# Kernel optimization log

Hardware: AMD Instinct MI355X
Metric: run time of the kernel (lower is better)

The kernel has to match this reference:

```python
import jax, jax.numpy as jnp
import numpy as np

B, S, N_CATE, N_CONT = 32, 1024, 4, 4
HIDDEN, ATTN, VOCAB, EMB = 1024, 512, 1000, 128


def sinusoidal_pe(seq_len, d_model, base=10000.0):
    pos = jnp.arange(seq_len, dtype=jnp.float32)[:, None]            # [S,1]
    i = jnp.arange(d_model // 2, dtype=jnp.float32)[None, :]         # [1,D/2]
    ang = pos / jnp.power(base, 2.0 * i / d_model)                   # [S,D/2]
    pe = jnp.zeros((seq_len, d_model), dtype=jnp.float32)
    pe = pe.at[:, 0::2].set(jnp.sin(ang))
    pe = pe.at[:, 1::2].set(jnp.cos(ang))
    return pe


def setup_inputs() -> dict:
    key = jax.random.key(0)
    ks = jax.random.split(key, 20)
    s = 0.02
    inp = {
        "cate_x": jax.random.randint(ks[0], (B, S, N_CATE), 0, VOCAB, dtype=jnp.int64)
                  if jax.config.read("jax_enable_x64") else
                  jax.random.randint(ks[0], (B, S, N_CATE), 0, VOCAB, dtype=jnp.int32),
        "cont_x": jax.random.normal(ks[1], (B, S, N_CONT), dtype=jnp.float32),
        "mask": jnp.ones((B, S), dtype=bool),
        "targets": jax.random.uniform(ks[2], (B, S), dtype=jnp.float32),
        # EntireEmbedding params: 4 cate tables + cont linear + comb projection
        "E0": jax.random.normal(ks[3], (VOCAB, EMB), dtype=jnp.float32) * s,
        "E1": jax.random.normal(ks[4], (VOCAB, EMB), dtype=jnp.float32) * s,
        "E2": jax.random.normal(ks[5], (VOCAB, EMB), dtype=jnp.float32) * s,
        "E3": jax.random.normal(ks[6], (VOCAB, EMB), dtype=jnp.float32) * s,
        "Wc": jax.random.normal(ks[7], (N_CONT, N_CATE * EMB), dtype=jnp.float32) * s,
        "Wproj": jax.random.normal(ks[8], (2 * N_CATE * EMB, HIDDEN), dtype=jnp.float32) * s,
        # two-head attention linears (bias=False)
        "WQ1": jax.random.normal(ks[9], (HIDDEN, ATTN), dtype=jnp.float32) * s,
        "WK1": jax.random.normal(ks[10], (HIDDEN, ATTN), dtype=jnp.float32) * s,
        "WV1": jax.random.normal(ks[11], (HIDDEN, ATTN), dtype=jnp.float32) * s,
        "WQ2": jax.random.normal(ks[12], (HIDDEN, ATTN), dtype=jnp.float32) * s,
        "WK2": jax.random.normal(ks[13], (HIDDEN, ATTN), dtype=jnp.float32) * s,
        "WV2": jax.random.normal(ks[14], (HIDDEN, ATTN), dtype=jnp.float32) * s,
        "W0": jax.random.normal(ks[15], (2 * ATTN, HIDDEN), dtype=jnp.float32) * s,
        "Wf": jax.random.normal(ks[16], (HIDDEN, 1), dtype=jnp.float32) * s,
    }
    return inp


def _attend(x, WQ, WK, WV):
    Q = x @ WQ  # [B,S,A]
    K = x @ WK
    V = x @ WV
    scores = jnp.einsum("bqd,bkd->bqk", Q, K) / jnp.sqrt(jnp.float32(ATTN))
    # faithful to nn.Softmax(dim=1): normalize over the QUERY axis
    attn = jax.nn.softmax(scores, axis=1)
    return jnp.einsum("bqk,bkv->bqv", attn, V)


def reference(cate_x, cont_x, mask, targets, E0, E1, E2, E3, Wc, Wproj,
              WQ1, WK1, WV1, WQ2, WK2, WV2, W0, Wf):
    # EntireEmbedding: per-feature cate embeddings + cont projection -> comb proj
    cate_emb = jnp.concatenate(
        [E0[cate_x[..., 0]], E1[cate_x[..., 1]], E2[cate_x[..., 2]], E3[cate_x[..., 3]]],
        axis=-1)                                   # [B,S,512]
    cont_emb = cont_x @ Wc                          # [B,S,512]
    x = jnp.concatenate([cate_emb, cont_emb], axis=-1) @ Wproj  # [B,S,H]
    x = x + sinusoidal_pe(x.shape[1], HIDDEN)[None, :, :]
    z1 = _attend(x, WQ1, WK1, WV1)                  # [B,S,A]
    z2 = _attend(x, WQ2, WK2, WV2)                  # [B,S,A]
    z = jnp.concatenate([z1, z2], axis=-1) @ W0     # [B,S,H]
    out = jax.nn.sigmoid(z @ Wf)                    # FinalConnecting: Linear(H,1)+sigmoid
    return out.squeeze(-1)                          # [B,S]
```

## Files before the change

kernel.cpp:

```cpp
#include <hip/hip_runtime.h>
#include <hip/hip_bf16.h>
#include <math.h>

#define BB    32
#define SS    1024
#define HID   1024
#define AT    512
#define NVOC  1000
#define NT    (BB*SS)

typedef unsigned short u16;
typedef __attribute__((ext_vector_type(8))) short s16x8;
typedef __attribute__((ext_vector_type(4))) float f32x4;

__device__ __forceinline__ float bf2f(u16 u) {
    union { unsigned int i; float f; } x; x.i = ((unsigned int)u) << 16; return x.f;
}
__device__ __forceinline__ u16 f2bf(float f) {
    union { float f; unsigned int i; } u; u.f = f;
    unsigned int r = u.i + 0x7fffu + ((u.i >> 16) & 1u);
    return (u16)(r >> 16);
}
__device__ __forceinline__ float4 ld4(const float* p) { return *(const float4*)p; }
__device__ __forceinline__ float4 ld4bf(const u16* p) {
    ushort4 v = *(const ushort4*)p;
    return make_float4(bf2f(v.x), bf2f(v.y), bf2f(v.z), bf2f(v.w));
}
__device__ __forceinline__ void unpack8(uint4 v, float* x) {
    x[0] = bf2f((u16)(v.x & 0xffff)); x[1] = bf2f((u16)(v.x >> 16));
    x[2] = bf2f((u16)(v.y & 0xffff)); x[3] = bf2f((u16)(v.y >> 16));
    x[4] = bf2f((u16)(v.z & 0xffff)); x[5] = bf2f((u16)(v.z >> 16));
    x[6] = bf2f((u16)(v.w & 0xffff)); x[7] = bf2f((u16)(v.w >> 16));
}

__device__ __forceinline__ void gld16(const u16* g, u16* l) {
    __builtin_amdgcn_global_load_lds(
        (const __attribute__((address_space(1))) unsigned int*)g,
        (__attribute__((address_space(3))) unsigned int*)l,
        16, 0, 0);
}

struct Ptrs4f { const float* p[4]; };

__device__ __forceinline__ float blockReduceSum(float x) {
    #pragma unroll
    for (int off = 32; off > 0; off >>= 1) x += __shfl_down(x, off, 64);
    __shared__ float tmp[4];
    int lane = threadIdx.x & 63, wid = threadIdx.x >> 6;
    if (lane == 0) tmp[wid] = x;
    __syncthreads();
    if (threadIdx.x == 0) x = tmp[0] + tmp[1] + tmp[2] + tmp[3];
    return x;
}
__device__ __forceinline__ float waveReduceSum(float x) {
    #pragma unroll
    for (int off = 32; off > 0; off >>= 1) x += __shfl_down(x, off, 64);
    return x;
}

__global__ void k_s1(Ptrs4f E, const float* __restrict__ Wproj, Ptrs4f W,
                     const float* __restrict__ W0, const float* __restrict__ Wf,
                     u16* __restrict__ PE16, u16* __restrict__ E16o, u16* __restrict__ Wp16,
                     u16* __restrict__ Wt, float* __restrict__ W0f,
                     float* __restrict__ Wcp, float* __restrict__ CQ) {
    int blk = blockIdx.x, tid = threadIdx.x;
    if (blk < 2048) {
        int idx = blk*256 + tid;
        int s = idx >> 9, i = idx & 511;
        const float l2_10000 = 13.287712379549449f;
        float denom = exp2f((2.f * (float)i / 1024.f) * l2_10000);
        float ang = (float)s / denom;
        unsigned int pack = ((unsigned int)f2bf(cosf(ang)) << 16) | f2bf(sinf(ang));
        *(unsigned int*)(PE16 + (size_t)s*1024 + 2*i) = pack;
    } else if (blk < 4048) {
        int id2 = blk - 2048;
        int f = id2 / 500;
        int i = (id2 % 500)*256 + tid;
        E16o[(size_t)f*128000 + i] = f2bf(E.p[f][i]);
    } else if (blk < 6096) {
        int i = (blk - 4048)*256 + tid;
        Wp16[i] = f2bf(Wproj[i]);
    } else if (blk < 8144) {
        int tb = blk - 6096;
        int mat = tb >> 9, t2 = tb & 511;
        int cx = t2 & 15, ry = t2 >> 4;
        int r0 = ry*32, c0 = cx*32;
        const float* in = W.p[mat];
        u16* out = Wt + (size_t)mat*1024*512;
        __shared__ float tt[32][33];
        int tx = tid & 31, ty8 = tid >> 5;
        #pragma unroll
        for (int it = 0; it < 4; ++it)
            tt[ty8 + it*8][tx] = in[(size_t)(r0 + ty8 + it*8)*512 + c0 + tx];
        __syncthreads();
        #pragma unroll
        for (int it = 0; it < 4; ++it)
            out[(size_t)(c0 + ty8 + it*8)*1024 + r0 + tx] = f2bf(tt[tx][ty8 + it*8]);
    } else if (blk < 9168) {
        int row = blk - 8144;
        const float* rp = W0 + (size_t)row*1024;
        float a = 0.f;
        for (int j = tid; j < 1024; j += 256) a += rp[j] * Wf[j];
        a = blockReduceSum(a);
        if (tid == 0) W0f[row] = a;
    } else {
        int idx = (blk - 9168)*256 + tid;
        if (idx < 4096) Wcp[idx] = 0.f;
        else CQ[idx - 4096] = 0.f;
    }
}

__global__ void k_s2(const float* __restrict__ Wc, const float* __restrict__ Wproj,
                     Ptrs4f W, const float* __restrict__ WV1, const float* __restrict__ WV2,
                     const float* __restrict__ W0f, float* __restrict__ Wcp, float* __restrict__ v) {
    int blk = blockIdx.x, tid = threadIdx.x;
    if (blk < 64) {
        int c = blk >> 4, ic = (blk >> 2) & 3, jc = blk & 3;
        int i = ic*256 + tid;
        float a = 0.f;
        for (int j = jc*128; j < jc*128 + 128; ++j)
            a += Wc[c*512 + j] * Wproj[(size_t)(512 + j)*1024 + i];
        atomicAdd(&Wcp[c*1024 + i], a);
    } else {
        int b2 = blk - 64;
        int h = b2 >> 10, i = b2 & 1023;
        const float* WV = h ? WV2 : WV1;
        const float* wf = W0f + h*512;
        float a = 0.f;
        for (int aa = tid; aa < 512; aa += 256) a += WV[(size_t)i*512 + aa] * wf[aa];
        a = blockReduceSum(a);
        if (tid == 0) v[h*1024 + i] = a;
    }
}

__device__ __forceinline__ void cstore(float* p, float v) { *p = v; }
__device__ __forceinline__ void cstore(u16* p, float v)   { *p = f2bf(v); }

template<typename CT, bool STATS, bool CTRANS>
__device__ __forceinline__ void mfma_gemm(const u16* __restrict__ A, const u16* __restrict__ B,
                                          CT* __restrict__ C, int M, int N, int K, float alpha,
                                          float* __restrict__ Pm, float* __restrict__ Pd,
                                          int m0, int n0) {
    __shared__ u16 As[128*64];
    __shared__ u16 Bs[128*64];
    const int tid = threadIdx.x;
    const int wave = tid >> 6, lane = tid & 63;
    const int quad = lane >> 4, l16 = lane & 15;
    const int wm = (wave >> 1)*64, wn = (wave & 1)*64;
    const int srow = lane >> 3;
    const int scol = ((lane & 7) ^ srow) * 8;
    f32x4 acc[4][4] = {};

    for (int k0 = 0; k0 < K; k0 += 64) {
        #pragma unroll
        for (int p = 0; p < 4; ++p) {
            int rb = wave*32 + p*8;
            gld16(A + (size_t)(m0 + rb + srow)*K + k0 + scol, As + rb*64);
            gld16(B + (size_t)(n0 + rb + srow)*K + k0 + scol, Bs + rb*64);
        }
        __syncthreads();
        #pragma unroll
        for (int kk = 0; kk < 2; ++kk) {
            s16x8 af[4], bf[4];
            #pragma unroll
            for (int i = 0; i < 4; ++i) {
                int row = wm + i*16 + l16;
                af[i] = *(const s16x8*)(As + row*64 + (((kk*4 + quad) ^ (row & 7)) * 8));
            }
            #pragma unroll
            for (int j = 0; j < 4; ++j) {
                int row = wn + j*16 + l16;
                bf[j] = *(const s16x8*)(Bs + row*64 + (((kk*4 + quad) ^ (row & 7)) * 8));
            }
            #pragma unroll
            for (int i = 0; i < 4; ++i)
                #pragma unroll
                for (int j = 0; j < 4; ++j)
                    acc[i][j] = __builtin_amdgcn_mfma_f32_16x16x32_bf16(af[i], bf[j], acc[i][j], 0, 0, 0);
        }
        __syncthreads();
    }
    if (STATS) {
        #pragma unroll
        for (int i = 0; i < 4; ++i)
            #pragma unroll
            for (int r = 0; r < 4; ++r) {
                int gm = m0 + wm + i*16 + quad*4 + r;
                u16 b0 = f2bf(acc[i][0][r] * alpha);
                u16 b1 = f2bf(acc[i][1][r] * alpha);
                u16 b2 = f2bf(acc[i][2][r] * alpha);
                u16 b3 = f2bf(acc[i][3][r] * alpha);
                acc[i][0][r] = bf2f(b0); acc[i][1][r] = bf2f(b1);
                acc[i][2][r] = bf2f(b2); acc[i][3][r] = bf2f(b3);
                unsigned int lo = (unsigned int)b0 | ((unsigned int)b1 << 16);
                unsigned int hi = (unsigned int)b2 | ((unsigned int)b3 << 16);
                *(uint2*)((u16*)C + (size_t)gm*N + n0 + wn + l16*4) = make_uint2(lo, hi);
            }
        __shared__ float sMax[4][64];
        __shared__ float sSum[4][64];
        #pragma unroll
        for (int j = 0; j < 4; ++j) {
            float mx = -3.4e38f;
            #pragma unroll
            for (int i = 0; i < 4; ++i)
                #pragma unroll
                for (int r = 0; r < 4; ++r) mx = fmaxf(mx, acc[i][j][r]);
            mx = fmaxf(mx, __shfl_xor(mx, 16, 64));
            mx = fmaxf(mx, __shfl_xor(mx, 32, 64));
            float sm = 0.f;
            #pragma unroll
            for (int i = 0; i < 4; ++i)
                #pragma unroll
                for (int r = 0; r < 4; ++r) sm += exp2f(acc[i][j][r] - mx);
            sm += __shfl_xor(sm, 16, 64);
            sm += __shfl_xor(sm, 32, 64);
            if (quad == 0) { sMax[wave][j*16 + l16] = mx; sSum[wave][j*16 + l16] = sm; }
        }
        __syncthreads();
        if (tid < 128) {
            int c = tid;
            int w0 = (c < 64) ? 0 : 1, ci = c & 63;
            float m0v = sMax[w0][ci],     s0 = sSum[w0][ci];
            float m1v = sMax[w0 + 2][ci], s1 = sSum[w0 + 2][ci];
            float mm = fmaxf(m0v, m1v);
            float ss = s0 * exp2f(m0v - mm) + s1 * exp2f(m1v - mm);
            Pm[n0 + c] = mm;
            Pd[n0 + c] = ss;
        }
    } else {
        #pragma unroll
        for (int i = 0; i < 4; ++i) {
            #pragma unroll
            for (int r = 0; r < 4; ++r) {
                int gm = m0 + wm + i*16 + quad*4 + r;
                if (gm < M) {
                    #pragma unroll
                    for (int j = 0; j < 4; ++j) {
                        int gn = n0 + wn + j*16 + l16;
                        if (CTRANS) cstore(C + (size_t)gn*M + gm, acc[i][j][r] * alpha);
                        else        cstore(C + (size_t)gm*N + gn, acc[i][j][r] * alpha);
                    }
                }
            }
        }
    }
}

__global__ __launch_bounds__(256) void k_s3(const u16* __restrict__ Wp16, const u16* __restrict__ Wt,
                                            u16* __restrict__ PWT,
                                            Ptrs4f W, const float* __restrict__ Wcp, float* __restrict__ CQ,
                                            const float* __restrict__ Wproj, const float* __restrict__ v,
                                            float* __restrict__ pv) {
    int blk = blockIdx.x, tid = threadIdx.x;
    if (blk < 64) {
        int x = blk & 3, z = blk >> 2;
        int f = z >> 2, w = z & 3;
        mfma_gemm<u16,false,true>(Wp16 + (size_t)f*128*1024, Wt + (size_t)w*512*1024,
                                  PWT + (size_t)z*512*128, 128, 512, 1024, 1.f,
                                  nullptr, nullptr, 0, x*128);
    } else if (blk < 320) {
        int r = blk - 64;
        int ns = r & 1, wc = (r >> 1) & 15, jc = r >> 5;
        int w = wc & 3, c = wc >> 2; int n = ns*256 + tid;
        const float* Ww = W.p[w];
        float a = 0.f;
        for (int j = jc*128; j < jc*128 + 128; ++j) a += Wcp[c*1024 + j] * Ww[(size_t)j*512 + n];
        atomicAdd(&CQ[(size_t)(w*4 + c)*512 + n], a);
    } else {
        int b2 = blk - 320;
        int i = b2 & 127, fh = b2 >> 7; int f = fh >> 1, h = fh & 1;
        const float* row = Wproj + (size_t)(f*128 + i)*1024;
        const float* vh = v + h*1024;
        float a = 0.f;
        for (int j = tid; j < 1024; j += 256) a += row[j] * vh[j];
        a = blockReduceSum(a);
        if (tid == 0) pv[(size_t)fh*128 + i] = a;
    }
}

__global__ __launch_bounds__(256) void k_s4(const u16* __restrict__ E16, const u16* __restrict__ PWT,
                                            const u16* __restrict__ PE16, const u16* __restrict__ Wt,
                                            u16* __restrict__ TQK16, u16* __restrict__ PEQ16,
                                            const float* __restrict__ Wcp, const float* __restrict__ v,
                                            const float* __restrict__ pv,
                                            float* __restrict__ Ut, float* __restrict__ pu, float* __restrict__ cu) {
    int blk = blockIdx.x;
    if (blk < 640) {
        int z = blk >> 5, r = blk & 31, y = r >> 2, x = r & 3;
        if (z < 16) {
            int f = z >> 2;
            mfma_gemm<u16,false,false>(E16 + (size_t)f*128000, PWT + (size_t)z*512*128,
                       TQK16 + (size_t)z*1000*512, 1000, 512, 128, 1.f, nullptr, nullptr,
                       y*128, x*128);
        } else {
            int w = z - 16;
            mfma_gemm<u16,false,false>(PE16, Wt + (size_t)w*512*1024, PEQ16 + (size_t)w*1024*512,
                       1024, 512, 1024, 1.f, nullptr, nullptr, y*128, x*128);
        }
        return;
    }
    int id = blk - 640;
    if (id < 2000) {
        int wave = threadIdx.x >> 6, lane = threadIdx.x & 63;
        int d = id*4 + wave;
        int f = d / 2000, h = (d / 1000) & 1, r = d % 1000;
        unsigned int e2 = *(const unsigned int*)(E16 + ((size_t)f*1000 + r)*128 + lane*2);
        const float* pvp = pv + (size_t)(f*2 + h)*128 + lane*2;
        float a = bf2f((u16)(e2 & 0xffff)) * pvp[0] + bf2f((u16)(e2 >> 16)) * pvp[1];
        a = waveReduceSum(a);
        if (lane == 0) Ut[(size_t)(f*2 + h)*1000 + r] = a;
    } else if (id < 4048) {
        int tq = id - 2000; int h = tq >> 10, s = tq & 1023;
        float4 a = ld4bf(PE16 + (size_t)s*1024 + threadIdx.x*4);
        float4 b = ld4(v + h*1024 + threadIdx.x*4);
        float p = a.x*b.x + a.y*b.y + a.z*b.z + a.w*b.w;
        p = blockReduceSum(p);
        if (threadIdx.x == 0) pu[h*1024 + s] = p;
    } else {
        int tq = id - 4048; int h = tq >> 2, c = tq & 3;
        float4 a = ld4(Wcp + c*1024 + threadIdx.x*4);
        float4 b = ld4(v + h*1024 + threadIdx.x*4);
        float p = a.x*b.x + a.y*b.y + a.z*b.z + a.w*b.w;
        p = blockReduceSum(p);
        if (threadIdx.x == 0) cu[h*4 + c] = p;
    }
}

__global__ __launch_bounds__(256, 6) void k_g_S(const u16* __restrict__ Q, const u16* __restrict__ K,
                                             u16* __restrict__ Sb, float alpha,
                                             float* __restrict__ Pm, float* __restrict__ Pd, int b0) {
    size_t b = blockIdx.z;
    int bx = (blockIdx.x % 4)*2 + (blockIdx.y % 2);
    int by = (blockIdx.x / 4)*4 + (blockIdx.y / 2);
    size_t po = ((b0 + b)*8 + by)*1024;
    mfma_gemm<u16,true,false>(Q + b*SS*AT, K + b*SS*AT, Sb + b*SS*SS, 1024, 1024, 512, alpha,
                        Pm + po, Pd + po, by*128, bx*128);
}

__global__ void k_gather(const int* __restrict__ cate, const float* __restrict__ cont,
                         const u16* __restrict__ TQK, const float* __restrict__ CQ,
                         const u16* __restrict__ PEQ, const float* __restrict__ Ut,
                         const float* __restrict__ cu, const float* __restrict__ pu,
                         u16* __restrict__ Qh, u16* __restrict__ Kh,
                         float* __restrict__ u, int h) {
    int tid = threadIdx.x;
    size_t t = (size_t)blockIdx.x*2 + (tid >> 7);
    int r = tid & 127;
    int s = (int)(t & 1023);
    int4 cc = *(const int4*)(cate + t*4);
    float4 cv = ld4(cont + t*4);
    int e = r >> 6;
    int w = 2*h + e;
    int n = (r & 63)*8;
    const u16* t0 = TQK + ((size_t)(0*4  + w)*1000 + cc.x)*512 + n;
    const u16* t1 = TQK + ((size_t)(1*4  + w)*1000 + cc.y)*512 + n;
    const u16* t2 = TQK + ((size_t)(2*4  + w)*1000 + cc.z)*512 + n;
    const u16* t3 = TQK + ((size_t)(3*4  + w)*1000 + cc.w)*512 + n;
    const u16* pq = PEQ + ((size_t)w*1024 + s)*512 + n;
    const float* cq = CQ + (size_t)w*2048 + n;
    float a0[8], a1[8], a2[8], a3[8], ap[8];
    unpack8(*(const uint4*)t0, a0); unpack8(*(const uint4*)t1, a1);
    unpack8(*(const uint4*)t2, a2); unpack8(*(const uint4*)t3, a3);
    unpack8(*(const uint4*)pq, ap);
    unsigned int pack[4];
    #pragma unroll
    for (int jp = 0; jp < 4; ++jp) {
        float x0, x1;
        #pragma unroll
        for (int half = 0; half < 2; ++half) {
            int j = jp*2 + half;
            float x = a0[j] + a1[j] + a2[j] + a3[j] + ap[j]
                    + cv.x*cq[j] + cv.y*cq[512+j] + cv.z*cq[1024+j] + cv.w*cq[1536+j];
            if (half == 0) x0 = x; else x1 = x;
        }
        pack[jp] = ((unsigned int)f2bf(x1) << 16) | f2bf(x0);
    }
    u16* op = (e ? Kh : Qh) + t*512 + n;
    *(uint4*)op = make_uint4(pack[0], pack[1], pack[2], pack[3]);
    if (r == 0) {
        float uu = pu[h*1024 + s]
                 + Ut[(0*2 + h)*1000 + cc.x] + Ut[(1*2 + h)*1000 + cc.y]
                 + Ut[(2*2 + h)*1000 + cc.z] + Ut[(3*2 + h)*1000 + cc.w]
                 + cv.x*cu[h*4+0] + cv.y*cu[h*4+1] + cv.z*cu[h*4+2] + cv.w*cu[h*4+3];
        u[(size_t)h*NT + t] = uu;
    }
}

__global__ void k_stats_combine(const float* __restrict__ Pm, const float* __restrict__ Pd,
                                const float* __restrict__ u, float* __restrict__ wexp, int b0) {
    int idx = b0*1024 + blockIdx.x*256 + threadIdx.x;
    int b = idx >> 10, k = idx & 1023;
    float mx = -3.4e38f;
    #pragma unroll
    for (int mt = 0; mt < 8; ++mt) mx = fmaxf(mx, Pm[((size_t)b*8 + mt)*1024 + k]);
    float dd = 0.f;
    #pragma unroll
    for (int mt = 0; mt < 8; ++mt) dd += Pd[((size_t)b*8 + mt)*1024 + k]
                                       * exp2f(Pm[((size_t)b*8 + mt)*1024 + k] - mx);
    int q = (k & ~63) | (((k & 15) << 2) | ((k & 63) >> 4));
    wexp[((size_t)b << 10) + q] = u[idx] / dd * exp2f(-mx);
}

__global__ void k_logit(const u16* __restrict__ Sb, const float* __restrict__ wexp,
                        float* __restrict__ logits, float* __restrict__ out,
                        int b0, int mode) {
    int wave = threadIdx.x >> 6, lane = threadIdx.x & 63;
    size_t bi = (size_t)(gridDim.x - 1 - blockIdx.x);
    size_t tl = bi*4 + wave;
    size_t tabs = (size_t)b0*1024 + tl;
    int b = (int)(tabs >> 10);
    const u16* row = Sb + tl*1024;
    const float* wb = wexp + ((size_t)b << 10);
    float acc = 0.f;
    #pragma unroll
    for (int half = 0; half < 2; ++half) {
        int k = lane*8 + half*512;
        float sv[8];
        unpack8(*(const uint4*)(row + k), sv);
        float4 w0 = ld4(wb + k), w1 = ld4(wb + k + 4);
        acc += exp2f(sv[0])*w0.x + exp2f(sv[1])*w0.y + exp2f(sv[2])*w0.z + exp2f(sv[3])*w0.w
             + exp2f(sv[4])*w1.x + exp2f(sv[5])*w1.y + exp2f(sv[6])*w1.z + exp2f(sv[7])*w1.w;
    }
    acc = waveReduceSum(acc);
    if (lane == 0) {
        if (mode == 0) logits[tabs] = acc;
        else {
            float x = logits[tabs] + acc;
            out[tabs] = 1.f / (1.f + expf(-x));
        }
    }
}

extern "C" void kernel_launch(void* const* d_in, const int* in_sizes, int n_in,
                              void* d_out, int out_size, void* d_ws, size_t ws_size,
                              hipStream_t stream) {
    const int*   cate = (const int*)d_in[0];
    const float* cont = (const float*)d_in[1];
    Ptrs4f E; E.p[0] = (const float*)d_in[4]; E.p[1] = (const float*)d_in[5];
              E.p[2] = (const float*)d_in[6]; E.p[3] = (const float*)d_in[7];
    const float* Wc    = (const float*)d_in[8];
    const float* Wproj = (const float*)d_in[9];
    Ptrs4f W; W.p[0] = (const float*)d_in[10];
              W.p[1] = (const float*)d_in[11];
              W.p[2] = (const float*)d_in[13];
              W.p[3] = (const float*)d_in[14];
    const float* WV1 = (const float*)d_in[12];
    const float* WV2 = (const float*)d_in[15];
    const float* W0  = (const float*)d_in[16];
    const float* Wf  = (const float*)d_in[17];

    char* base = (char*)d_ws;
    size_t off = 0;
    auto alloc = [&](size_t bytes) { void* p = base + off; off += (bytes + 255) & ~(size_t)255; return p; };
    u16*   PE16  = (u16*)  alloc(1048576ull*2);
    u16*   E16   = (u16*)  alloc(4ull*1000*128*2);
    u16*   Wt    = (u16*)  alloc(4ull*512*1024*2);
    u16*   Wp16  = (u16*)  alloc(512ull*1024*2);
    u16*   PWT   = (u16*)  alloc(16ull*512*128*2);
    u16*   TQK16 = (u16*)  alloc(16ull*1000*512*2);
    u16*   PEQ16 = (u16*)  alloc(4ull*1024*512*2);
    float* Wcp   = (float*)alloc(4*1024*4);
    float* W0f   = (float*)alloc(1024*4);
    float* vv    = (float*)alloc(2*1024*4);
    float* CQ    = (float*)alloc(16*512*4);
    float* pvb   = (float*)alloc(8*128*4);
    float* Ut    = (float*)alloc(8*1000*4);
    float* cu    = (float*)alloc(8*4);
    float* pu    = (float*)alloc(2*1024*4);
    float* ubuf  = (float*)alloc(2ull*NT*4);
    u16*   Qh    = (u16*)  alloc((size_t)NT*512*2);
    u16*   Kh    = (u16*)  alloc((size_t)NT*512*2);
    float* Pm    = (float*)alloc(32ull*8*1024*4);
    float* Pd    = (float*)alloc(32ull*8*1024*4);
    float* wbuf  = (float*)alloc(32*1024*4);
    float* logits= (float*)alloc((size_t)NT*4);
    size_t sChunkBytes = (size_t)SS*SS*2;
    size_t remain = (ws_size > off) ? (ws_size - off) : 0;
    int NB = (int)(remain / sChunkBytes);
    if (NB > 32) NB = 32;
    if (NB < 1) NB = 1;
    u16* Sbuf = (u16*)(base + off);

    const float alpha = 0.06375954951107036f;

    k_s1<<<9216, 256, 0, stream>>>(E, Wproj, W, W0, Wf, PE16, E16, Wp16, Wt, W0f, Wcp, CQ);
    k_s2<<<2112, 256, 0, stream>>>(Wc, Wproj, W, WV1, WV2, W0f, Wcp, vv);
    k_s3<<<1344, 256, 0, stream>>>(Wp16, Wt, PWT, W, Wcp, CQ, Wproj, vv, pvb);
    k_s4<<<4696, 256, 0, stream>>>(E16, PWT, PE16, Wt, TQK16, PEQ16, Wcp, vv, pvb, Ut, pu, cu);

    for (int h = 0; h < 2; ++h) {
        k_gather<<<NT/2, 256, 0, stream>>>(cate, cont, TQK16, CQ, PEQ16, Ut, cu, pu, Qh, Kh, ubuf, h);
        for (int b0 = 0; b0 < 32; b0 += NB) {
            int nb = (32 - b0 < NB) ? (32 - b0) : NB;
            k_g_S<<<dim3(8, 8, nb), 256, 0, stream>>>(Qh + (size_t)b0*SS*AT, Kh + (size_t)b0*SS*AT, Sbuf, alpha, Pm, Pd, b0);
            k_stats_combine<<<nb*4, 256, 0, stream>>>(Pm, Pd, ubuf + (size_t)h*NT, wbuf, b0);
            k_logit<<<nb*256, 256, 0, stream>>>(Sbuf, wbuf, logits, (float*)d_out, b0, h);
        }
    }
}
```

Measured before the change: 377.4 us.

## Replace score GEMM with 256x256-tile double-buffered kernel and XCD-aware block swizzle

The per-batch Q·K^T score GEMM moves from 128x128 tiles with 256 threads to a dedicated 256x256-tile kernel with 512 threads. It double-buffers the LDS tiles with explicit vmcnt waits, raises wave priority around the MFMA bursts, and remaps block IDs so neighbouring tiles land on the same XCD. Column softmax partial stats are now produced per 256-row tile, so the combine kernel reads 4 partials instead of 8. The aim is more operand reuse per load and overlap of global loads with MFMA work. The cost is higher register and LDS pressure (128 KB shared) and fewer blocks per batch chunk.

```diff
diff --git a/kernel.cpp b/kernel.cpp
--- a/kernel.cpp
+++ b/kernel.cpp
@@ -136,10 +136,9 @@
 __device__ __forceinline__ void cstore(float* p, float v) { *p = v; }
 __device__ __forceinline__ void cstore(u16* p, float v)   { *p = f2bf(v); }
 
-template<typename CT, bool STATS, bool CTRANS>
+template<typename CT, bool CTRANS>
 __device__ __forceinline__ void mfma_gemm(const u16* __restrict__ A, const u16* __restrict__ B,
                                           CT* __restrict__ C, int M, int N, int K, float alpha,
-                                          float* __restrict__ Pm, float* __restrict__ Pd,
                                           int m0, int n0) {
     __shared__ u16 As[128*64];
     __shared__ u16 Bs[128*64];
@@ -180,66 +179,17 @@
         }
         __syncthreads();
     }
-    if (STATS) {
-        #pragma unroll
-        for (int i = 0; i < 4; ++i)
-            #pragma unroll
-            for (int r = 0; r < 4; ++r) {
-                int gm = m0 + wm + i*16 + quad*4 + r;
-                u16 b0 = f2bf(acc[i][0][r] * alpha);
-                u16 b1 = f2bf(acc[i][1][r] * alpha);
-                u16 b2 = f2bf(acc[i][2][r] * alpha);
-                u16 b3 = f2bf(acc[i][3][r] * alpha);
-                acc[i][0][r] = bf2f(b0); acc[i][1][r] = bf2f(b1);
-                acc[i][2][r] = bf2f(b2); acc[i][3][r] = bf2f(b3);
-                unsigned int lo = (unsigned int)b0 | ((unsigned int)b1 << 16);
-                unsigned int hi = (unsigned int)b2 | ((unsigned int)b3 << 16);
-                *(uint2*)((u16*)C + (size_t)gm*N + n0 + wn + l16*4) = make_uint2(lo, hi);
-            }
-        __shared__ float sMax[4][64];
-        __shared__ float sSum[4][64];
-        #pragma unroll
-        for (int j = 0; j < 4; ++j) {
-            float mx = -3.4e38f;
-            #pragma unroll
-            for (int i = 0; i < 4; ++i)
+    #pragma unroll
+    for (int i = 0; i < 4; ++i) {
+        #pragma unroll
+        for (int r = 0; r < 4; ++r) {
+            int gm = m0 + wm + i*16 + quad*4 + r;
+            if (gm < M) {
                 #pragma unroll
-                for (int r = 0; r < 4; ++r) mx = fmaxf(mx, acc[i][j][r]);
-            mx = fmaxf(mx, __shfl_xor(mx, 16, 64));
-            mx = fmaxf(mx, __shfl_xor(mx, 32, 64));
-            float sm = 0.f;
-            #pragma unroll
-            for (int i = 0; i < 4; ++i)
-                #pragma unroll
-                for (int r = 0; r < 4; ++r) sm += exp2f(acc[i][j][r] - mx);
-            sm += __shfl_xor(sm, 16, 64);
-            sm += __shfl_xor(sm, 32, 64);
-            if (quad == 0) { sMax[wave][j*16 + l16] = mx; sSum[wave][j*16 + l16] = sm; }
-        }
-        __syncthreads();
-        if (tid < 128) {
-            int c = tid;
-            int w0 = (c < 64) ? 0 : 1, ci = c & 63;
-            float m0v = sMax[w0][ci],     s0 = sSum[w0][ci];
-            float m1v = sMax[w0 + 2][ci], s1 = sSum[w0 + 2][ci];
-            float mm = fmaxf(m0v, m1v);
-            float ss = s0 * exp2f(m0v - mm) + s1 * exp2f(m1v - mm);
-            Pm[n0 + c] = mm;
-            Pd[n0 + c] = ss;
-        }
-    } else {
-        #pragma unroll
-        for (int i = 0; i < 4; ++i) {
-            #pragma unroll
-            for (int r = 0; r < 4; ++r) {
-                int gm = m0 + wm + i*16 + quad*4 + r;
-                if (gm < M) {
-                    #pragma unroll
-                    for (int j = 0; j < 4; ++j) {
-                        int gn = n0 + wn + j*16 + l16;
-                        if (CTRANS) cstore(C + (size_t)gn*M + gm, acc[i][j][r] * alpha);
-                        else        cstore(C + (size_t)gm*N + gn, acc[i][j][r] * alpha);
-                    }
+                for (int j = 0; j < 4; ++j) {
+                    int gn = n0 + wn + j*16 + l16;
+                    if (CTRANS) cstore(C + (size_t)gn*M + gm, acc[i][j][r] * alpha);
+                    else        cstore(C + (size_t)gm*N + gn, acc[i][j][r] * alpha);
                 }
             }
         }
@@ -255,9 +205,8 @@
     if (blk < 64) {
         int x = blk & 3, z = blk >> 2;
         int f = z >> 2, w = z & 3;
-        mfma_gemm<u16,false,true>(Wp16 + (size_t)f*128*1024, Wt + (size_t)w*512*1024,
-                                  PWT + (size_t)z*512*128, 128, 512, 1024, 1.f,
-                                  nullptr, nullptr, 0, x*128);
+        mfma_gemm<u16,true>(Wp16 + (size_t)f*128*1024, Wt + (size_t)w*512*1024,
+                            PWT + (size_t)z*512*128, 128, 512, 1024, 1.f, 0, x*128);
     } else if (blk < 320) {
         int r = blk - 64;
         int ns = r & 1, wc = (r >> 1) & 15, jc = r >> 5;
@@ -289,13 +238,12 @@
         int z = blk >> 5, r = blk & 31, y = r >> 2, x = r & 3;
         if (z < 16) {
             int f = z >> 2;
-            mfma_gemm<u16,false,false>(E16 + (size_t)f*128000, PWT + (size_t)z*512*128,
-                       TQK16 + (size_t)z*1000*512, 1000, 512, 128, 1.f, nullptr, nullptr,
-                       y*128, x*128);
+            mfma_gemm<u16,false>(E16 + (size_t)f*128000, PWT + (size_t)z*512*128,
+                       TQK16 + (size_t)z*1000*512, 1000, 512, 128, 1.f, y*128, x*128);
         } else {
             int w = z - 16;
-            mfma_gemm<u16,false,false>(PE16, Wt + (size_t)w*512*1024, PEQ16 + (size_t)w*1024*512,
-                       1024, 512, 1024, 1.f, nullptr, nullptr, y*128, x*128);
+            mfma_gemm<u16,false>(PE16, Wt + (size_t)w*512*1024, PEQ16 + (size_t)w*1024*512,
+                       1024, 512, 1024, 1.f, y*128, x*128);
         }
         return;
     }
@@ -326,15 +274,145 @@
     }
 }
 
-__global__ __launch_bounds__(256, 6) void k_g_S(const u16* __restrict__ Q, const u16* __restrict__ K,
-                                             u16* __restrict__ Sb, float alpha,
-                                             float* __restrict__ Pm, float* __restrict__ Pd, int b0) {
-    size_t b = blockIdx.z;
-    int bx = (blockIdx.x % 4)*2 + (blockIdx.y % 2);
-    int by = (blockIdx.x / 4)*4 + (blockIdx.y / 2);
-    size_t po = ((b0 + b)*8 + by)*1024;
-    mfma_gemm<u16,true,false>(Q + b*SS*AT, K + b*SS*AT, Sb + b*SS*SS, 1024, 1024, 512, alpha,
-                        Pm + po, Pd + po, by*128, bx*128);
+__global__ __launch_bounds__(512, 2) void k_g_S256(
+        const u16* __restrict__ Q, const u16* __restrict__ K,
+        u16* __restrict__ Sb, float alpha,
+        float* __restrict__ Pm, float* __restrict__ Pd, int b0) {
+    __shared__ u16 As[2][16384];
+    __shared__ u16 Bs[2][16384];
+    const int tid = threadIdx.x;
+    const int wave = tid >> 6, lane = tid & 63;
+    const int quad = lane >> 4, l16 = lane & 15;
+    const int wm = wave >> 2, wn = wave & 3;
+
+    const int nwg = (int)gridDim.x;
+    int fblk = (int)blockIdx.x;
+    int qq = nwg >> 3, rr = nwg & 7;
+    int xcd = fblk & 7, idx = fblk >> 3;
+    int swz = (xcd < rr ? xcd*(qq + 1) : rr*(qq + 1) + (xcd - rr)*qq) + idx;
+    int b = swz >> 4, tile = swz & 15;
+    int m0 = (tile >> 2) << 8, n0 = (tile & 3) << 8;
+
+    const u16* __restrict__ Ab = Q + (size_t)b*SS*AT;
+    const u16* __restrict__ Bb = K + (size_t)b*SS*AT;
+    u16* __restrict__ C = Sb + (size_t)b*SS*SS;
+
+    const int srow = lane >> 3;
+    const int scol = ((lane & 7) ^ srow) * 8;
+
+    f32x4 acc[8][4] = {};
+
+    auto stage = [&](int kt, int bf) {
+        const u16* ap = Ab + (size_t)(m0 + wave*8 + srow)*AT + kt*64 + scol;
+        const u16* bp = Bb + (size_t)(n0 + wave*8 + srow)*AT + kt*64 + scol;
+        u16* la = &As[bf][wave*8*64];
+        u16* lb = &Bs[bf][wave*8*64];
+        #pragma unroll
+        for (int p = 0; p < 4; ++p) {
+            gld16(ap + (size_t)p*64*AT, la + p*64*64);
+            gld16(bp + (size_t)p*64*AT, lb + p*64*64);
+        }
+    };
+
+    auto compute = [&](int bf) {
+        s16x8 bfr[4][2];
+        #pragma unroll
+        for (int j = 0; j < 4; ++j) {
+            int row = wn*64 + j*16 + l16;
+            #pragma unroll
+            for (int kk = 0; kk < 2; ++kk)
+                bfr[j][kk] = *(const s16x8*)(&Bs[bf][row*64 + (((kk*4 + quad) ^ (row & 7)) * 8)]);
+        }
+        #pragma unroll
+        for (int ib = 0; ib < 2; ++ib) {
+            s16x8 afr[4][2];
+            #pragma unroll
+            for (int i2 = 0; i2 < 4; ++i2) {
+                int row = wm*128 + (ib*4 + i2)*16 + l16;
+                #pragma unroll
+                for (int kk = 0; kk < 2; ++kk)
+                    afr[i2][kk] = *(const s16x8*)(&As[bf][row*64 + (((kk*4 + quad) ^ (row & 7)) * 8)]);
+            }
+            __builtin_amdgcn_s_setprio(1);
+            #pragma unroll
+            for (int i2 = 0; i2 < 4; ++i2) {
+                #pragma unroll
+                for (int j = 0; j < 4; ++j) {
+                    acc[ib*4+i2][j] = __builtin_amdgcn_mfma_f32_16x16x32_bf16(afr[i2][0], bfr[j][0], acc[ib*4+i2][j], 0, 0, 0);
+                    acc[ib*4+i2][j] = __builtin_amdgcn_mfma_f32_16x16x32_bf16(afr[i2][1], bfr[j][1], acc[ib*4+i2][j], 0, 0, 0);
+                }
+            }
+            __builtin_amdgcn_s_setprio(0);
+        }
+    };
+
+    stage(0, 0);
+    stage(1, 1);
+    asm volatile("s_waitcnt vmcnt(8)" ::: "memory");
+    __builtin_amdgcn_s_barrier();
+
+    #pragma unroll
+    for (int t = 0; t < 8; ++t) {
+        compute(t & 1);
+        asm volatile("" ::: "memory");
+        __builtin_amdgcn_s_barrier();
+        if (t < 6) {
+            stage(t + 2, t & 1);
+            asm volatile("s_waitcnt vmcnt(8)" ::: "memory");
+        } else if (t == 6) {
+            asm volatile("s_waitcnt vmcnt(0)" ::: "memory");
+        }
+        __builtin_amdgcn_sched_barrier(0);
+        __builtin_amdgcn_s_barrier();
+    }
+
+    #pragma unroll
+    for (int i = 0; i < 8; ++i) {
+        #pragma unroll
+        for (int r = 0; r < 4; ++r) {
+            int gm = m0 + wm*128 + i*16 + quad*4 + r;
+            u16 q0 = f2bf(acc[i][0][r] * alpha);
+            u16 q1 = f2bf(acc[i][1][r] * alpha);
+            u16 q2 = f2bf(acc[i][2][r] * alpha);
+            u16 q3 = f2bf(acc[i][3][r] * alpha);
+            acc[i][0][r] = bf2f(q0); acc[i][1][r] = bf2f(q1);
+            acc[i][2][r] = bf2f(q2); acc[i][3][r] = bf2f(q3);
+            unsigned int lo = (unsigned int)q0 | ((unsigned int)q1 << 16);
+            unsigned int hi = (unsigned int)q2 | ((unsigned int)q3 << 16);
+            *(uint2*)(C + (size_t)gm*SS + n0 + wn*64 + l16*4) = make_uint2(lo, hi);
+        }
+    }
+    float* sM = (float*)&As[0][0];
+    float* sS = (float*)&Bs[0][0];
+    #pragma unroll
+    for (int j = 0; j < 4; ++j) {
+        float mx = -3.4e38f;
+        #pragma unroll
+        for (int i = 0; i < 8; ++i)
+            #pragma unroll
+            for (int r = 0; r < 4; ++r) mx = fmaxf(mx, acc[i][j][r]);
+        mx = fmaxf(mx, __shfl_xor(mx, 16, 64));
+        mx = fmaxf(mx, __shfl_xor(mx, 32, 64));
+        float sm = 0.f;
+        #pragma unroll
+        for (int i = 0; i < 8; ++i)
+            #pragma unroll
+            for (int r = 0; r < 4; ++r) sm += exp2f(acc[i][j][r] - mx);
+        sm += __shfl_xor(sm, 16, 64);
+        sm += __shfl_xor(sm, 32, 64);
+        if (quad == 0) { sM[wave*64 + j*16 + l16] = mx; sS[wave*64 + j*16 + l16] = sm; }
+    }
+    __syncthreads();
+    if (tid < 256) {
+        int c = tid, wq = c >> 6, cc = c & 63;
+        float ma = sM[wq*64 + cc],       sa = sS[wq*64 + cc];
+        float mb = sM[(4 + wq)*64 + cc], sb2 = sS[(4 + wq)*64 + cc];
+        float mm = fmaxf(ma, mb);
+        float ss = sa * exp2f(ma - mm) + sb2 * exp2f(mb - mm);
+        size_t po = ((size_t)(b0 + b)*4 + (m0 >> 8))*1024;
+        Pm[po + n0 + c] = mm;
+        Pd[po + n0 + c] = ss;
+    }
 }
 
 __global__ void k_gather(const int* __restrict__ cate, const float* __restrict__ cont,
@@ -392,11 +470,11 @@
     int b = idx >> 10, k = idx & 1023;
     float mx = -3.4e38f;
     #pragma unroll
-    for (int mt = 0; mt < 8; ++mt) mx = fmaxf(mx, Pm[((size_t)b*8 + mt)*1024 + k]);
+    for (int mt = 0; mt < 4; ++mt) mx = fmaxf(mx, Pm[((size_t)b*4 + mt)*1024 + k]);
     float dd = 0.f;
     #pragma unroll
-    for (int mt = 0; mt < 8; ++mt) dd += Pd[((size_t)b*8 + mt)*1024 + k]
-                                       * exp2f(Pm[((size_t)b*8 + mt)*1024 + k] - mx);
+    for (int mt = 0; mt < 4; ++mt) dd += Pd[((size_t)b*4 + mt)*1024 + k]
+                                       * exp2f(Pm[((size_t)b*4 + mt)*1024 + k] - mx);
     int q = (k & ~63) | (((k & 15) << 2) | ((k & 63) >> 4));
     wexp[((size_t)b << 10) + q] = u[idx] / dd * exp2f(-mx);
 }
@@ -492,7 +570,8 @@
         k_gather<<<NT/2, 256, 0, stream>>>(cate, cont, TQK16, CQ, PEQ16, Ut, cu, pu, Qh, Kh, ubuf, h);
         for (int b0 = 0; b0 < 32; b0 += NB) {
             int nb = (32 - b0 < NB) ? (32 - b0) : NB;
-            k_g_S<<<dim3(8, 8, nb), 256, 0, stream>>>(Qh + (size_t)b0*SS*AT, Kh + (size_t)b0*SS*AT, Sbuf, alpha, Pm, Pd, b0);
+            k_g_S256<<<16*nb, 512, 0, stream>>>(Qh + (size_t)b0*SS*AT, Kh + (size_t)b0*SS*AT,
+                                                Sbuf, alpha, Pm, Pd, b0);
             k_stats_combine<<<nb*4, 256, 0, stream>>>(Pm, Pd, ubuf + (size_t)h*NT, wbuf, b0);
             k_logit<<<nb*256, 256, 0, stream>>>(Sbuf, wbuf, logits, (float*)d_out, b0, h);
         }
```

After: 365.3 us. 1.03x faster.
